# Kernel tuning notes

Hardware: AMD Instinct MI355X
Metric: run time of the kernel (lower is better)

Reference implementation:

```python
import jax, jax.numpy as jnp
import numpy as np

WS = 8      # window size
NH = 8      # num heads
DIM = 256
SHIFT = WS // 2  # shift=True path


def _relative_position_index(ws):
    coords = np.stack(np.meshgrid(np.arange(ws), np.arange(ws), indexing='ij'))  # [2,ws,ws]
    cf = coords.reshape(2, -1)
    rel = cf[:, :, None] - cf[:, None, :]            # [2,ws*ws,ws*ws]
    rel = rel.transpose(1, 2, 0)
    rel[:, :, 0] += ws - 1
    rel[:, :, 1] += ws - 1
    rel[:, :, 0] *= 2 * ws - 1
    return rel.sum(-1).astype(np.int32)              # [ws*ws,ws*ws]


def setup_inputs() -> dict:
    key = jax.random.key(0)
    ks = jax.random.split(key, 7)
    B, H, W, C = 2, 256, 256, DIM
    x = jax.random.normal(ks[0], (B, H, W, C), dtype=jnp.float32)
    qkv_w = jax.random.normal(ks[1], (3 * C, C), dtype=jnp.float32) * 0.02
    qkv_b = jnp.zeros((3 * C,), dtype=jnp.float32)
    proj_w = jax.random.normal(ks[2], (C, C), dtype=jnp.float32) * 0.02
    proj_b = jnp.zeros((C,), dtype=jnp.float32)
    bias_table = jax.random.normal(ks[3], ((2 * WS - 1) ** 2, NH), dtype=jnp.float32) * 0.02
    rel_index = jnp.asarray(_relative_position_index(WS))
    return {"x": x, "qkv_w": qkv_w, "qkv_b": qkv_b, "proj_w": proj_w,
            "proj_b": proj_b, "bias_table": bias_table, "rel_index": rel_index}


def reference(x, qkv_w, qkv_b, proj_w, proj_b, bias_table, rel_index):
    B, H, W, C = x.shape
    ws, nh = WS, NH
    hd = C // nh
    scale = hd ** -0.5
    n = ws * ws
    # cyclic shift
    x = jnp.roll(x, shift=(-SHIFT, -SHIFT), axis=(1, 2))
    # window partition -> [B*nW, ws*ws, C]
    xw = x.reshape(B, H // ws, ws, W // ws, ws, C)
    xw = xw.transpose(0, 1, 3, 2, 4, 5).reshape(-1, n, C)
    # qkv projection (torch Linear: y = x @ W.T + b)
    qkv = xw @ qkv_w.T + qkv_b
    qkv = qkv.reshape(-1, n, 3, nh, hd).transpose(2, 0, 3, 1, 4)  # [3, nW, nh, n, hd]
    q, k, v = qkv[0] * scale, qkv[1], qkv[2]
    attn = jnp.einsum('whid,whjd->whij', q, k)  # [nW, nh, n, n]
    bias = bias_table[rel_index.reshape(-1)].reshape(n, n, nh).transpose(2, 0, 1)
    attn = jax.nn.softmax(attn + bias[None], axis=-1)
    out = jnp.einsum('whij,whjd->whid', attn, v)               # [nW, nh, n, hd]
    out = out.transpose(0, 2, 1, 3).reshape(-1, n, C)
    out = out @ proj_w.T + proj_b
    # window reverse
    out = out.reshape(B, H // ws, W // ws, ws, ws, C)
    out = out.transpose(0, 1, 3, 2, 4, 5).reshape(B, H, W, C)
    return jnp.roll(out, shift=(SHIFT, SHIFT), axis=(1, 2))
```

## Files before the change

### kernel.cpp

```cpp
#include <hip/hip_runtime.h>
#include <hip/hip_bf16.h>

typedef _Float16 f16;
typedef _Float16 f16x8 __attribute__((ext_vector_type(8)));
typedef _Float16 f16x4 __attribute__((ext_vector_type(4)));
typedef float f32x4 __attribute__((ext_vector_type(4)));

#define SCALE 0.17677669529663687f

#define QW_OFF   0
#define PW_OFF   393216
#define QB_OFF   524288
#define BF_OFF   527360

#define SW(row, col) (((row) << 8) + ((col) ^ (((row) & 7) << 3)))

__global__ __launch_bounds__(256) void prep_kernel(
    const float* __restrict__ qkv_w, const float* __restrict__ qkv_b,
    const float* __restrict__ proj_w, const float* __restrict__ bias_table,
    const int* __restrict__ rel_index,
    f16* __restrict__ qw_h, f16* __restrict__ pw_h,
    float* __restrict__ qb_s, float* __restrict__ bias_fr) {
  int i = blockIdx.x * 256 + threadIdx.x;
  if (i < 768 * 256) {
    float s = (i < 256 * 256) ? SCALE : 1.0f;
    qw_h[i] = (f16)(qkv_w[i] * s);
  }
  if (i < 768) qb_s[i] = qkv_b[i] * (i < 256 ? SCALE : 1.0f);
  if (i < 256 * 256) pw_h[i] = (f16)proj_w[i];
  if (i < 8 * 4 * 4 * 256) {
    int h = i >> 12, rest = i & 4095;
    int qt = rest >> 10, kt = (rest >> 8) & 3, l = (rest >> 2) & 63, r = i & 3;
    int q = qt * 16 + (l & 15);
    int ke = kt * 16 + 4 * (l >> 4) + r;
    bias_fr[i] = bias_table[rel_index[q * 64 + ke] * 8 + h];
  }
}

__global__ __launch_bounds__(256, 2) void fused_kernel(
    const float* __restrict__ x, const f16* __restrict__ qw_h,
    const float* __restrict__ qb_s, const float* __restrict__ bias_fr,
    const f16* __restrict__ pw_h, const float* __restrict__ proj_b,
    float* __restrict__ out) {

  __shared__ f16 sx[64 * 256];
  __shared__ f16 stg[4][2304];

  const int tid = threadIdx.x;
  const int lane = tid & 63;
  const int wv = tid >> 6;
  const int lo = lane & 15, hi = lane >> 4;

  const int win = blockIdx.x;
  const int b = win >> 10, wh = (win >> 5) & 31, ww = win & 31;

  {
    const int t = tid >> 2, q4 = tid & 3;
    const int r = t >> 3, c = t & 7;
    const int gr = (wh * 8 + r + 4) & 255;
    const int gc = (ww * 8 + c + 4) & 255;
    const float* src = x + (((size_t)(b * 256 + gr)) * 256 + gc) * 256;
#pragma unroll
    for (int i = 0; i < 8; ++i) {
      const int off = q4 * 8 + i * 32;
      float4 v0 = *(const float4*)(src + off);
      float4 v1 = *(const float4*)(src + off + 4);
      f16x8 hv;
      hv[0] = (f16)v0.x; hv[1] = (f16)v0.y; hv[2] = (f16)v0.z; hv[3] = (f16)v0.w;
      hv[4] = (f16)v1.x; hv[5] = (f16)v1.y; hv[6] = (f16)v1.z; hv[7] = (f16)v1.w;
      *(f16x8*)&sx[SW(t, off)] = hv;
    }
  }
  __syncthreads();

  f16* ws_ = &stg[wv][0];
  f16x8 qf[2][4];
  f16x8 kf[2][4];
  f16x8 vf[2][2][2];

#pragma unroll
  for (int bn = 0; bn < 3; ++bn) {
    const int fwave = bn * 256 + wv * 64;

    f32x4 acc[4][4];
#pragma unroll
    for (int nt = 0; nt < 4; ++nt)
#pragma unroll
      for (int mt = 0; mt < 4; ++mt) acc[nt][mt] = (f32x4){0.f, 0.f, 0.f, 0.f};

    f16x8 bf[2][4];
#pragma unroll
    for (int nt = 0; nt < 4; ++nt)
      bf[0][nt] = *(const f16x8*)&qw_h[(size_t)(fwave + nt * 16 + lo) * 256 + 8 * hi];

#pragma unroll
    for (int kt = 0; kt < 8; ++kt) {
      const int cur = kt & 1;
      if (kt < 7) {
#pragma unroll
        for (int nt = 0; nt < 4; ++nt)
          bf[cur ^ 1][nt] = *(const f16x8*)&qw_h[(size_t)(fwave + nt * 16 + lo) * 256 + (kt + 1) * 32 + 8 * hi];
      }
      f16x8 a[4];
#pragma unroll
      for (int mt = 0; mt < 4; ++mt)
        a[mt] = *(const f16x8*)&sx[SW(mt * 16 + lo, kt * 32 + 8 * hi)];
#pragma unroll
      for (int nt = 0; nt < 4; ++nt)
#pragma unroll
        for (int mt = 0; mt < 4; ++mt) {
          if (bn < 2)
            acc[nt][mt] = __builtin_amdgcn_mfma_f32_16x16x32_f16(bf[cur][nt], a[mt], acc[nt][mt], 0, 0, 0);
          else
            acc[nt][mt] = __builtin_amdgcn_mfma_f32_16x16x32_f16(a[mt], bf[cur][nt], acc[nt][mt], 0, 0, 0);
        }
    }

    if (bn < 2) {
#pragma unroll
      for (int hsel = 0; hsel < 2; ++hsel) {
#pragma unroll
        for (int h2 = 0; h2 < 2; ++h2) {
#pragma unroll
          for (int n2 = 0; n2 < 2; ++n2) {
            const int nt = hsel * 2 + n2;
            const f32x4 bias4 = *(const f32x4*)&qb_s[fwave + nt * 16 + 4 * hi];
#pragma unroll
            for (int mtl = 0; mtl < 2; ++mtl) {
              const int mt = h2 * 2 + mtl;
              f16x4 t;
#pragma unroll
              for (int r4 = 0; r4 < 4; ++r4) t[r4] = (f16)(acc[nt][mt][r4] + bias4[r4]);
              *(f16x4*)&ws_[(mtl * 16 + lo) * 40 + n2 * 16 + 4 * hi] = t;
            }
          }
#pragma unroll
          for (int t4l = 0; t4l < 2; ++t4l) {
            f16x8 fr = *(const f16x8*)&ws_[(t4l * 16 + lo) * 40 + 8 * hi];
            if (bn == 0) qf[hsel][h2 * 2 + t4l] = fr;
            else         kf[hsel][h2 * 2 + t4l] = fr;
          }
        }
      }
    } else {
#pragma unroll
      for (int hsel = 0; hsel < 2; ++hsel) {
#pragma unroll
        for (int n2 = 0; n2 < 2; ++n2) {
          const int nt = hsel * 2 + n2;
          const float bias = qb_s[fwave + nt * 16 + lo];
#pragma unroll
          for (int mt = 0; mt < 4; ++mt) {
            f16x4 t;
#pragma unroll
            for (int r4 = 0; r4 < 4; ++r4) t[r4] = (f16)(acc[nt][mt][r4] + bias);
            *(f16x4*)&ws_[(n2 * 16 + lo) * 72 + mt * 16 + 4 * hi] = t;
          }
        }
#pragma unroll
        for (int kk = 0; kk < 2; ++kk)
#pragma unroll
          for (int dt = 0; dt < 2; ++dt)
            vf[hsel][kk][dt] = *(const f16x8*)&ws_[(dt * 16 + lo) * 72 + kk * 32 + 8 * hi];
      }
    }
  }

  __syncthreads();
  f16* sao = sx;
  const f32x4 zero = {0.f, 0.f, 0.f, 0.f};
  f16x8 vone;
#pragma unroll
  for (int j = 0; j < 8; ++j) vone[j] = (f16)1.0f;

#pragma unroll
  for (int hsel = 0; hsel < 2; ++hsel) {
    const int h = 2 * wv + hsel;
#pragma unroll
    for (int qh = 0; qh < 2; ++qh) {
      f32x4 s[2][4];
#pragma unroll
      for (int q2 = 0; q2 < 2; ++q2)
#pragma unroll
        for (int kt = 0; kt < 4; ++kt)
          s[q2][kt] = *(const f32x4*)&bias_fr[(((h * 4 + qh * 2 + q2) * 4 + kt) << 8) + lane * 4];
#pragma unroll
      for (int q2 = 0; q2 < 2; ++q2)
#pragma unroll
        for (int kt = 0; kt < 4; ++kt)
          s[q2][kt] = __builtin_amdgcn_mfma_f32_16x16x32_f16(kf[hsel][kt], qf[hsel][qh * 2 + q2], s[q2][kt], 0, 0, 0);

#pragma unroll
      for (int q2 = 0; q2 < 2; ++q2)
#pragma unroll
        for (int kt = 0; kt < 4; ++kt) {
          f16x4 t;
#pragma unroll
          for (int r4 = 0; r4 < 4; ++r4) t[r4] = (f16)__expf(s[q2][kt][r4]);
          *(f16x4*)&ws_[(q2 * 16 + lo) * 72 + kt * 16 + 4 * hi] = t;
        }

      f32x4 o[2][2], oa[2];
#pragma unroll
      for (int q2 = 0; q2 < 2; ++q2) {
        oa[q2] = zero;
#pragma unroll
        for (int dt = 0; dt < 2; ++dt) o[q2][dt] = zero;
      }
#pragma unroll
      for (int kk = 0; kk < 2; ++kk) {
        f16x8 pB[2];
#pragma unroll
        for (int q2 = 0; q2 < 2; ++q2)
          pB[q2] = *(const f16x8*)&ws_[(q2 * 16 + lo) * 72 + kk * 32 + 8 * hi];
#pragma unroll
        for (int q2 = 0; q2 < 2; ++q2) {
          oa[q2] = __builtin_amdgcn_mfma_f32_16x16x32_f16(vone, pB[q2], oa[q2], 0, 0, 0);
#pragma unroll
          for (int dt = 0; dt < 2; ++dt)
            o[q2][dt] = __builtin_amdgcn_mfma_f32_16x16x32_f16(vf[hsel][kk][dt], pB[q2], o[q2][dt], 0, 0, 0);
        }
      }

#pragma unroll
      for (int q2 = 0; q2 < 2; ++q2) {
        const float inv = __builtin_amdgcn_rcpf(oa[q2][0]);
        const int tok = qh * 32 + q2 * 16 + lo;
#pragma unroll
        for (int dt = 0; dt < 2; ++dt) {
          f16x4 t;
#pragma unroll
          for (int r4 = 0; r4 < 4; ++r4) t[r4] = (f16)(o[q2][dt][r4] * inv);
          *(f16x4*)&sao[SW(tok, h * 32 + dt * 16 + 4 * hi)] = t;
        }
      }
    }
  }

  __syncthreads();

  f32x4 acc[4][4];
#pragma unroll
  for (int j = 0; j < 4; ++j)
#pragma unroll
    for (int mt = 0; mt < 4; ++mt) acc[j][mt] = (f32x4){0.f, 0.f, 0.f, 0.f};

  f16x8 bfp[2][4];
#pragma unroll
  for (int j = 0; j < 4; ++j)
    bfp[0][j] = *(const f16x8*)&pw_h[(size_t)((4 * wv + j) * 16 + lo) * 256 + 8 * hi];

#pragma unroll
  for (int kt = 0; kt < 8; ++kt) {
    const int cur = kt & 1;
    if (kt < 7) {
#pragma unroll
      for (int j = 0; j < 4; ++j)
        bfp[cur ^ 1][j] = *(const f16x8*)&pw_h[(size_t)((4 * wv + j) * 16 + lo) * 256 + (kt + 1) * 32 + 8 * hi];
    }
    f16x8 a[4];
#pragma unroll
    for (int mt = 0; mt < 4; ++mt)
      a[mt] = *(const f16x8*)&sao[SW(mt * 16 + lo, kt * 32 + 8 * hi)];
#pragma unroll
    for (int j = 0; j < 4; ++j)
#pragma unroll
      for (int mt = 0; mt < 4; ++mt)
        acc[j][mt] = __builtin_amdgcn_mfma_f32_16x16x32_f16(a[mt], bfp[cur][j], acc[j][mt], 0, 0, 0);
  }

#pragma unroll
  for (int j = 0; j < 4; ++j) {
    const int n = (4 * wv + j) * 16 + lo;
    const float pb = proj_b[n];
#pragma unroll
    for (int mt = 0; mt < 4; ++mt)
#pragma unroll
      for (int r4 = 0; r4 < 4; ++r4) {
        const int token = mt * 16 + 4 * hi + r4;
        const int tr = token >> 3, tc = token & 7;
        const int gr = (wh * 8 + tr + 4) & 255;
        const int gc = (ww * 8 + tc + 4) & 255;
        out[(((size_t)(b * 256 + gr)) * 256 + gc) * 256 + n] = acc[j][mt][r4] + pb;
      }
  }
}

extern "C" void kernel_launch(void* const* d_in, const int* in_sizes, int n_in,
                              void* d_out, int out_size, void* d_ws, size_t ws_size,
                              hipStream_t stream) {
  const float* x          = (const float*)d_in[0];
  const float* qkv_w      = (const float*)d_in[1];
  const float* qkv_b      = (const float*)d_in[2];
  const float* proj_w     = (const float*)d_in[3];
  const float* proj_b     = (const float*)d_in[4];
  const float* bias_table = (const float*)d_in[5];
  const int*   rel_index  = (const int*)d_in[6];
  float* out = (float*)d_out;

  char* ws = (char*)d_ws;
  f16*   qw_h    = (f16*)(ws + QW_OFF);
  f16*   pw_h    = (f16*)(ws + PW_OFF);
  float* qb_s    = (float*)(ws + QB_OFF);
  float* bias_fr = (float*)(ws + BF_OFF);

  prep_kernel<<<768, 256, 0, stream>>>(qkv_w, qkv_b, proj_w, bias_table, rel_index,
                                       qw_h, pw_h, qb_s, bias_fr);
  fused_kernel<<<2048, 256, 0, stream>>>(x, qw_h, qb_s, bias_fr, pw_h, proj_b, out);
}
```

Baseline: 176.1 us.

## Use 8 waves per window block, one attention head per wave

The fused kernel now runs with 512 threads (8 waves) per window instead of 256. Each wave handles a single head and 32 output columns in the QKV and projection GEMMs, rather than two heads and 64 columns. This halves the per-wave accumulator and fragment registers so more waves can be resident, which should help hide latency. The cost is more LDS staging per block (8 staging buffers), the same per-block LDS for x, and smaller per-wave MFMA tiles with less register reuse of the A fragments.

```diff
diff --git a/kernel.cpp b/kernel.cpp
--- a/kernel.cpp
+++ b/kernel.cpp
@@ -37,14 +37,14 @@
   }
 }
 
-__global__ __launch_bounds__(256, 2) void fused_kernel(
+__global__ __launch_bounds__(512, 4) void fused_kernel(
     const float* __restrict__ x, const f16* __restrict__ qw_h,
     const float* __restrict__ qb_s, const float* __restrict__ bias_fr,
     const f16* __restrict__ pw_h, const float* __restrict__ proj_b,
     float* __restrict__ out) {
 
   __shared__ f16 sx[64 * 256];
-  __shared__ f16 stg[4][2304];
+  __shared__ f16 stg[8][2304];
 
   const int tid = threadIdx.x;
   const int lane = tid & 63;
@@ -55,14 +55,14 @@
   const int b = win >> 10, wh = (win >> 5) & 31, ww = win & 31;
 
   {
-    const int t = tid >> 2, q4 = tid & 3;
+    const int t = tid >> 3, q8 = tid & 7;
     const int r = t >> 3, c = t & 7;
     const int gr = (wh * 8 + r + 4) & 255;
     const int gc = (ww * 8 + c + 4) & 255;
     const float* src = x + (((size_t)(b * 256 + gr)) * 256 + gc) * 256;
 #pragma unroll
-    for (int i = 0; i < 8; ++i) {
-      const int off = q4 * 8 + i * 32;
+    for (int i = 0; i < 4; ++i) {
+      const int off = q8 * 32 + i * 8;
       float4 v0 = *(const float4*)(src + off);
       float4 v1 = *(const float4*)(src + off + 4);
       f16x8 hv;
@@ -74,39 +74,39 @@
   __syncthreads();
 
   f16* ws_ = &stg[wv][0];
-  f16x8 qf[2][4];
-  f16x8 kf[2][4];
-  f16x8 vf[2][2][2];
+  f16x8 qf[4];
+  f16x8 kf[4];
+  f16x8 vf[2][2];
 
 #pragma unroll
   for (int bn = 0; bn < 3; ++bn) {
-    const int fwave = bn * 256 + wv * 64;
-
-    f32x4 acc[4][4];
-#pragma unroll
-    for (int nt = 0; nt < 4; ++nt)
+    const int f0 = bn * 256 + wv * 32;
+
+    f32x4 acc[2][4];
+#pragma unroll
+    for (int nt = 0; nt < 2; ++nt)
 #pragma unroll
       for (int mt = 0; mt < 4; ++mt) acc[nt][mt] = (f32x4){0.f, 0.f, 0.f, 0.f};
 
-    f16x8 bf[2][4];
-#pragma unroll
-    for (int nt = 0; nt < 4; ++nt)
-      bf[0][nt] = *(const f16x8*)&qw_h[(size_t)(fwave + nt * 16 + lo) * 256 + 8 * hi];
+    f16x8 bf[2][2];
+#pragma unroll
+    for (int nt = 0; nt < 2; ++nt)
+      bf[0][nt] = *(const f16x8*)&qw_h[(size_t)(f0 + nt * 16 + lo) * 256 + 8 * hi];
 
 #pragma unroll
     for (int kt = 0; kt < 8; ++kt) {
       const int cur = kt & 1;
       if (kt < 7) {
 #pragma unroll
-        for (int nt = 0; nt < 4; ++nt)
-          bf[cur ^ 1][nt] = *(const f16x8*)&qw_h[(size_t)(fwave + nt * 16 + lo) * 256 + (kt + 1) * 32 + 8 * hi];
+        for (int nt = 0; nt < 2; ++nt)
+          bf[cur ^ 1][nt] = *(const f16x8*)&qw_h[(size_t)(f0 + nt * 16 + lo) * 256 + (kt + 1) * 32 + 8 * hi];
       }
       f16x8 a[4];
 #pragma unroll
       for (int mt = 0; mt < 4; ++mt)
         a[mt] = *(const f16x8*)&sx[SW(mt * 16 + lo, kt * 32 + 8 * hi)];
 #pragma unroll
-      for (int nt = 0; nt < 4; ++nt)
+      for (int nt = 0; nt < 2; ++nt)
 #pragma unroll
         for (int mt = 0; mt < 4; ++mt) {
           if (bn < 2)
@@ -118,51 +118,43 @@
 
     if (bn < 2) {
 #pragma unroll
-      for (int hsel = 0; hsel < 2; ++hsel) {
-#pragma unroll
-        for (int h2 = 0; h2 < 2; ++h2) {
-#pragma unroll
-          for (int n2 = 0; n2 < 2; ++n2) {
-            const int nt = hsel * 2 + n2;
-            const f32x4 bias4 = *(const f32x4*)&qb_s[fwave + nt * 16 + 4 * hi];
-#pragma unroll
-            for (int mtl = 0; mtl < 2; ++mtl) {
-              const int mt = h2 * 2 + mtl;
-              f16x4 t;
-#pragma unroll
-              for (int r4 = 0; r4 < 4; ++r4) t[r4] = (f16)(acc[nt][mt][r4] + bias4[r4]);
-              *(f16x4*)&ws_[(mtl * 16 + lo) * 40 + n2 * 16 + 4 * hi] = t;
-            }
+      for (int h2 = 0; h2 < 2; ++h2) {
+#pragma unroll
+        for (int nt = 0; nt < 2; ++nt) {
+          const f32x4 bias4 = *(const f32x4*)&qb_s[f0 + nt * 16 + 4 * hi];
+#pragma unroll
+          for (int mtl = 0; mtl < 2; ++mtl) {
+            const int mt = h2 * 2 + mtl;
+            f16x4 t;
+#pragma unroll
+            for (int r4 = 0; r4 < 4; ++r4) t[r4] = (f16)(acc[nt][mt][r4] + bias4[r4]);
+            *(f16x4*)&ws_[(mtl * 16 + lo) * 40 + nt * 16 + 4 * hi] = t;
           }
-#pragma unroll
-          for (int t4l = 0; t4l < 2; ++t4l) {
-            f16x8 fr = *(const f16x8*)&ws_[(t4l * 16 + lo) * 40 + 8 * hi];
-            if (bn == 0) qf[hsel][h2 * 2 + t4l] = fr;
-            else         kf[hsel][h2 * 2 + t4l] = fr;
-          }
+        }
+#pragma unroll
+        for (int t4l = 0; t4l < 2; ++t4l) {
+          f16x8 fr = *(const f16x8*)&ws_[(t4l * 16 + lo) * 40 + 8 * hi];
+          if (bn == 0) qf[h2 * 2 + t4l] = fr;
+          else         kf[h2 * 2 + t4l] = fr;
         }
       }
     } else {
 #pragma unroll
-      for (int hsel = 0; hsel < 2; ++hsel) {
-#pragma unroll
-        for (int n2 = 0; n2 < 2; ++n2) {
-          const int nt = hsel * 2 + n2;
-          const float bias = qb_s[fwave + nt * 16 + lo];
-#pragma unroll
-          for (int mt = 0; mt < 4; ++mt) {
-            f16x4 t;
-#pragma unroll
-            for (int r4 = 0; r4 < 4; ++r4) t[r4] = (f16)(acc[nt][mt][r4] + bias);
-            *(f16x4*)&ws_[(n2 * 16 + lo) * 72 + mt * 16 + 4 * hi] = t;
-          }
-        }
-#pragma unroll
-        for (int kk = 0; kk < 2; ++kk)
-#pragma unroll
-          for (int dt = 0; dt < 2; ++dt)
-            vf[hsel][kk][dt] = *(const f16x8*)&ws_[(dt * 16 + lo) * 72 + kk * 32 + 8 * hi];
-      }
+      for (int nt = 0; nt < 2; ++nt) {
+        const float bias = qb_s[f0 + nt * 16 + lo];
+#pragma unroll
+        for (int mt = 0; mt < 4; ++mt) {
+          f16x4 t;
+#pragma unroll
+          for (int r4 = 0; r4 < 4; ++r4) t[r4] = (f16)(acc[nt][mt][r4] + bias);
+          *(f16x4*)&ws_[(nt * 16 + lo) * 72 + mt * 16 + 4 * hi] = t;
+        }
+      }
+#pragma unroll
+      for (int kk = 0; kk < 2; ++kk)
+#pragma unroll
+        for (int dt = 0; dt < 2; ++dt)
+          vf[kk][dt] = *(const f16x8*)&ws_[(dt * 16 + lo) * 72 + kk * 32 + 8 * hi];
     }
   }
 
@@ -173,9 +165,8 @@
 #pragma unroll
   for (int j = 0; j < 8; ++j) vone[j] = (f16)1.0f;
 
-#pragma unroll
-  for (int hsel = 0; hsel < 2; ++hsel) {
-    const int h = 2 * wv + hsel;
+  {
+    const int h = wv;
 #pragma unroll
     for (int qh = 0; qh < 2; ++qh) {
       f32x4 s[2][4];
@@ -188,7 +179,7 @@
       for (int q2 = 0; q2 < 2; ++q2)
 #pragma unroll
         for (int kt = 0; kt < 4; ++kt)
-          s[q2][kt] = __builtin_amdgcn_mfma_f32_16x16x32_f16(kf[hsel][kt], qf[hsel][qh * 2 + q2], s[q2][kt], 0, 0, 0);
+          s[q2][kt] = __builtin_amdgcn_mfma_f32_16x16x32_f16(kf[kt], qf[qh * 2 + q2], s[q2][kt], 0, 0, 0);
 
 #pragma unroll
       for (int q2 = 0; q2 < 2; ++q2)
@@ -218,7 +209,7 @@
           oa[q2] = __builtin_amdgcn_mfma_f32_16x16x32_f16(vone, pB[q2], oa[q2], 0, 0, 0);
 #pragma unroll
           for (int dt = 0; dt < 2; ++dt)
-            o[q2][dt] = __builtin_amdgcn_mfma_f32_16x16x32_f16(vf[hsel][kk][dt], pB[q2], o[q2][dt], 0, 0, 0);
+            o[q2][dt] = __builtin_amdgcn_mfma_f32_16x16x32_f16(vf[kk][dt], pB[q2], o[q2][dt], 0, 0, 0);
         }
       }
 
@@ -239,39 +230,39 @@
 
   __syncthreads();
 
-  f32x4 acc[4][4];
-#pragma unroll
-  for (int j = 0; j < 4; ++j)
+  f32x4 acc[2][4];
+#pragma unroll
+  for (int j = 0; j < 2; ++j)
 #pragma unroll
     for (int mt = 0; mt < 4; ++mt) acc[j][mt] = (f32x4){0.f, 0.f, 0.f, 0.f};
 
-  f16x8 bfp[2][4];
-#pragma unroll
-  for (int j = 0; j < 4; ++j)
-    bfp[0][j] = *(const f16x8*)&pw_h[(size_t)((4 * wv + j) * 16 + lo) * 256 + 8 * hi];
+  f16x8 bfp[2][2];
+#pragma unroll
+  for (int j = 0; j < 2; ++j)
+    bfp[0][j] = *(const f16x8*)&pw_h[(size_t)(wv * 32 + j * 16 + lo) * 256 + 8 * hi];
 
 #pragma unroll
   for (int kt = 0; kt < 8; ++kt) {
     const int cur = kt & 1;
     if (kt < 7) {
 #pragma unroll
-      for (int j = 0; j < 4; ++j)
-        bfp[cur ^ 1][j] = *(const f16x8*)&pw_h[(size_t)((4 * wv + j) * 16 + lo) * 256 + (kt + 1) * 32 + 8 * hi];
+      for (int j = 0; j < 2; ++j)
+        bfp[cur ^ 1][j] = *(const f16x8*)&pw_h[(size_t)(wv * 32 + j * 16 + lo) * 256 + (kt + 1) * 32 + 8 * hi];
     }
     f16x8 a[4];
 #pragma unroll
     for (int mt = 0; mt < 4; ++mt)
       a[mt] = *(const f16x8*)&sao[SW(mt * 16 + lo, kt * 32 + 8 * hi)];
 #pragma unroll
-    for (int j = 0; j < 4; ++j)
+    for (int j = 0; j < 2; ++j)
 #pragma unroll
       for (int mt = 0; mt < 4; ++mt)
         acc[j][mt] = __builtin_amdgcn_mfma_f32_16x16x32_f16(a[mt], bfp[cur][j], acc[j][mt], 0, 0, 0);
   }
 
 #pragma unroll
-  for (int j = 0; j < 4; ++j) {
-    const int n = (4 * wv + j) * 16 + lo;
+  for (int j = 0; j < 2; ++j) {
+    const int n = wv * 32 + j * 16 + lo;
     const float pb = proj_b[n];
 #pragma unroll
     for (int mt = 0; mt < 4; ++mt)
@@ -306,5 +297,5 @@
 
   prep_kernel<<<768, 256, 0, stream>>>(qkv_w, qkv_b, proj_w, bias_table, rel_index,
                                        qw_h, pw_h, qb_s, bias_fr);
-  fused_kernel<<<2048, 256, 0, stream>>>(x, qw_h, qb_s, bias_fr, pw_h, proj_b, out);
+  fused_kernel<<<2048, 512, 0, stream>>>(x, qw_h, qb_s, bias_fr, pw_h, proj_b, out);
 }
```

Result: faster. 167.7 us (-4.8%).
